# Performance work log

Hardware: AMD Instinct MI355X
Metric: run time of the kernel (lower is better)

The kernel has to match this reference:

```python
import jax, jax.numpy as jnp
import numpy as np

B, IN, OUT, M = 4096, 512, 512, 16


def setup_inputs() -> dict:
    key = jax.random.key(0)
    k1, k2, k3 = jax.random.split(key, 3)
    # inputs kept strictly positive and inside the physical range [0, 60]
    x = jax.random.uniform(k1, (B, IN), jnp.float32, 0.1, 10.0)
    # photonic basis coefficients: positive, with small polynomial terms
    b_coef = jax.random.uniform(k2, (M, 8), jnp.float32, 0.1, 0.9)
    b_coef = b_coef.at[:, 4:].multiply(0.01)
    coeffs = 0.01 * jax.random.normal(k3, (OUT, IN, M), jnp.float32)
    return {"x": x, "coeffs": coeffs, "b_coef": b_coef}


def _photonic_basis(x, b):
    # x: (B, IN) -> broadcast against M basis functions -> (B, IN, M)
    xe = x[:, :, None]                                   # (B, IN, 1)
    b1, b2, b3, b4, b5, b6, b7, b8 = [b[:, i][None, None, :] for i in range(8)]
    inner = jnp.expm1(b3 * xe)
    powered = jnp.power(inner, b4)
    y = (b1 * jnp.log(1.0 + b2 * jnp.log1p(powered))
         + b5 * xe + b6 * xe**2 + b7 * xe**3 + b8 * xe**4)
    return y


def reference(x, coeffs, b_coef):
    # basis: (B, IN, M); double reduce over (IN, M) == GEMM of size B x (IN*M) x OUT
    basis = _photonic_basis(x, b_coef)
    y = jnp.einsum('bim,oim->bo', basis, coeffs)         # (B, OUT)
    return y
```

## Files before the change

kernel.cpp:

```cpp
#include <hip/hip_runtime.h>
#include <hip/hip_bf16.h>
#include <stdint.h>

#define B_DIM   4096
#define IN_DIM  512
#define OUT_DIM 512
#define M_DIM   16
#define K_DIM   (IN_DIM * M_DIM)
#define MN      (B_DIM * OUT_DIM)

typedef unsigned short ushort_t;
typedef __attribute__((ext_vector_type(8))) __bf16 bf16x8;
typedef __attribute__((ext_vector_type(2))) __bf16 bf16x2;
typedef __attribute__((ext_vector_type(4))) float  f32x4;

__device__ __forceinline__ ushort_t f2bf(float f) {
  union { float f; uint32_t u; } v; v.f = f;
  uint32_t u = v.u + 0x7fffu + ((v.u >> 16) & 1u);
  return (ushort_t)(u >> 16);
}

__device__ __forceinline__ uint32_t pkbf(float lo, float hi) {
  union { bf16x2 h; uint32_t u; } v;
  v.h[0] = (__bf16)lo; v.h[1] = (__bf16)hi;
  return v.u;
}

__device__ __forceinline__ float rfl(float f) {
  union { float f; int i; } v; v.f = f;
  v.i = __builtin_amdgcn_readfirstlane(v.i);
  return v.f;
}

#define CONV_N4 (OUT_DIM * K_DIM / 4)
__global__ __launch_bounds__(256) void convert_coeffs_kernel(
    const float* __restrict__ src, ushort_t* __restrict__ dst) {
  int i = blockIdx.x * 256 + threadIdx.x;
  float4 v = ((const float4*)src)[i];
  ushort4 o;
  o.x = f2bf(v.x); o.y = f2bf(v.y); o.z = f2bf(v.z); o.w = f2bf(v.w);
  ((ushort4*)dst)[i] = o;
}

#define BM 128
#define BN 512
#define BK 32
#define SPLITK 8
#define KC (K_DIM / SPLITK)
#define NITER (KC / BK)
#define XCOLS (KC / M_DIM)
#define XPAD  129

#define GLD16(g, l) \
  __builtin_amdgcn_global_load_lds((const __attribute__((address_space(1))) void*)(g), \
                                   (__attribute__((address_space(3))) void*)(l), 16, 0, 0)

template <int ATOMIC>
__global__ __launch_bounds__(512, 2) void gemm_kernel(
    const float* __restrict__ x,
    const ushort_t* __restrict__ Bt,
    const float* __restrict__ bc,
    float* __restrict__ P) {
  __shared__ __align__(16) ushort_t As[2][BM * BK];
  __shared__ __align__(16) ushort_t Bs[2][BN * BK];
  __shared__ __align__(16) float    Xs[XCOLS * XPAD];
  const int tid  = threadIdx.x;
  const int wave = tid >> 6;
  const int lane = tid & 63;
  const int wgid = blockIdx.x;
  const int ks = wgid & 7, bm = wgid >> 3;

  {
    const int r = tid >> 2, q = tid & 3;
    const float4* xrow = (const float4*)(x + (size_t)(bm * BM + r) * IN_DIM + ks * XCOLS);
    #pragma unroll
    for (int j = 0; j < 4; ++j) {
      float4 v = xrow[q * 4 + j];
      Xs[(q * 16 + j * 4 + 0) * XPAD + r] = v.x;
      Xs[(q * 16 + j * 4 + 1) * XPAD + r] = v.y;
      Xs[(q * 16 + j * 4 + 2) * XPAD + r] = v.z;
      Xs[(q * 16 + j * 4 + 3) * XPAD + r] = v.w;
    }
  }

  const int srow = wave * 16 + (lane >> 2);
  const int scol = (((lane & 3) ^ ((lane >> 3) & 3)) * 8);
  const ushort_t* Bg0 = Bt + (size_t)srow * K_DIM + ks * KC + scol;
  const ushort_t* Bg1 = Bg0 + (size_t)128 * K_DIM;
  const ushort_t* Bg2 = Bg0 + (size_t)256 * K_DIM;
  const ushort_t* Bg3 = Bg0 + (size_t)384 * K_DIM;
  const int bofs0 = (wave * 16) * BK;
  const int bofs1 = (128 + wave * 16) * BK;
  const int bofs2 = (256 + wave * 16) * BK;
  const int bofs3 = (384 + wave * 16) * BK;

#define STAGEB(b) do { \
    GLD16(Bg0, &Bs[b][bofs0]); GLD16(Bg1, &Bs[b][bofs1]); \
    GLD16(Bg2, &Bs[b][bofs2]); GLD16(Bg3, &Bs[b][bofs3]); \
    Bg0 += BK; Bg1 += BK; Bg2 += BK; Bg3 += BK; } while (0)

  const int half = wave & 1;
  const int arow = (wave >> 1) * 32 + (lane >> 1);
  const int il   = lane & 1;
  const int aslot = ((il * 2 + half) ^ ((lane >> 2) & 3));
  const int awe   = arow * BK + aslot * 8;
  const int xbase = il * XPAD + arow;

  float c1[8], c2[8], c3[8], c4[8], c5[8], c6[8], c7[8], c8[8];
  {
    const float* bch = bc + half * 64;
    #pragma unroll
    for (int m = 0; m < 8; ++m) {
      c1[m] = rfl(bch[m*8+0]); c2[m] = rfl(bch[m*8+1]);
      c3[m] = rfl(bch[m*8+2]); c4[m] = rfl(bch[m*8+3]);
      c5[m] = rfl(bch[m*8+4]); c6[m] = rfl(bch[m*8+5]);
      c7[m] = rfl(bch[m*8+6]); c8[m] = rfl(bch[m*8+7]);
    }
  }

  const float LOG2E = 1.44269504088896340736f;
  const float LN2   = 0.69314718055994530942f;
#define BASIS(b, t) do { \
    float xv = Xs[xbase + 2 * XPAD * (t)]; \
    float xl2 = xv * LOG2E; \
    float x2 = xv * xv, x3 = x2 * xv, x4 = x2 * x2; \
    float ym[8]; \
    _Pragma("unroll") \
    for (int mi = 0; mi < 8; ++mi) { \
      float e     = __builtin_amdgcn_exp2f(c3[mi] * xl2); \
      float inner = e - 1.0f; \
      float p     = __builtin_amdgcn_exp2f(c4[mi] * __builtin_amdgcn_logf(inner)); \
      float u     = LN2 * __builtin_amdgcn_logf(1.0f + p); \
      float vv    = LN2 * __builtin_amdgcn_logf(1.0f + c2[mi] * u); \
      ym[mi] = c1[mi] * vv + c5[mi] * xv + c6[mi] * x2 + c7[mi] * x3 + c8[mi] * x4; \
    } \
    *(uint4*)&As[b][awe] = make_uint4(pkbf(ym[0], ym[1]), pkbf(ym[2], ym[3]), \
                                      pkbf(ym[4], ym[5]), pkbf(ym[6], ym[7])); \
  } while (0)

  const int wr = wave >> 2, wc = wave & 3;
  const int fm = lane & 15;
  const int fkswz = (((lane >> 4) ^ ((lane >> 1) & 3)) << 3);

  f32x4 acc[4][8] = {};

#define COMPUTE(b) do { \
    bf16x8 af[4], bfv[8]; \
    _Pragma("unroll") \
    for (int t2 = 0; t2 < 4; ++t2) \
      af[t2] = *(const bf16x8*)&As[b][(wr * 64 + t2 * 16 + fm) * BK + fkswz]; \
    _Pragma("unroll") \
    for (int u = 0; u < 8; ++u) \
      bfv[u] = *(const bf16x8*)&Bs[b][(wc * 128 + u * 16 + fm) * BK + fkswz]; \
    __builtin_amdgcn_s_setprio(1); \
    _Pragma("unroll") \
    for (int mt = 0; mt < 4; ++mt) \
      _Pragma("unroll") \
      for (int nt = 0; nt < 8; ++nt) \
        acc[mt][nt] = __builtin_amdgcn_mfma_f32_16x16x32_bf16(af[mt], bfv[nt], acc[mt][nt], 0, 0, 0); \
    __builtin_amdgcn_s_setprio(0); \
  } while (0)

  STAGEB(0);
  __syncthreads();
  BASIS(0, 0);
  __syncthreads();
  for (int kt = 0; kt < NITER - 2; kt += 2) {
    STAGEB(1); COMPUTE(0); BASIS(1, kt + 1);
    __syncthreads();
    STAGEB(0); COMPUTE(1); BASIS(0, kt + 2);
    __syncthreads();
  }
  STAGEB(1); COMPUTE(0); BASIS(1, NITER - 1);
  __syncthreads();
  COMPUTE(1);

  const int colb = wc * 128 + fm;
  const int rowb = bm * BM + wr * 64 + (lane >> 4) * 4;
  float* out = P + (ATOMIC ? (size_t)0 : (size_t)ks * MN);
  #pragma unroll
  for (int mt = 0; mt < 4; ++mt) {
    #pragma unroll
    for (int nt = 0; nt < 8; ++nt) {
      #pragma unroll
      for (int j = 0; j < 4; ++j) {
        int row = rowb + mt * 16 + j;
        int col = colb + nt * 16;
        float vv = acc[mt][nt][j];
        if (ATOMIC) atomicAdd(out + (size_t)row * OUT_DIM + col, vv);
        else        out[(size_t)row * OUT_DIM + col] = vv;
      }
    }
  }
#undef STAGEB
#undef BASIS
#undef COMPUTE
}

__global__ __launch_bounds__(256) void reduce_kernel(
    const float* __restrict__ P, float* __restrict__ out) {
  int i = blockIdx.x * 256 + threadIdx.x;
  const float4* p = (const float4*)P;
  float4 r = p[i];
  #pragma unroll
  for (int s = 1; s < SPLITK; ++s) {
    float4 v = p[i + (size_t)s * (MN / 4)];
    r.x += v.x; r.y += v.y; r.z += v.z; r.w += v.w;
  }
  ((float4*)out)[i] = r;
}

extern "C" void kernel_launch(void* const* d_in, const int* in_sizes, int n_in,
                              void* d_out, int out_size, void* d_ws, size_t ws_size,
                              hipStream_t stream) {
  const float* x      = (const float*)d_in[0];
  const float* coeffs = (const float*)d_in[1];
  const float* b_coef = (const float*)d_in[2];
  float* out = (float*)d_out;
  char*  ws  = (char*)d_ws;

  const size_t COEF_BYTES = (size_t)OUT_DIM * K_DIM * 2;
  ushort_t* coefb = (ushort_t*)ws;
  float* partials = (float*)(ws + COEF_BYTES);
  const size_t FULL = COEF_BYTES + (size_t)SPLITK * MN * 4;
  const bool use_atomic = (ws_size < FULL);

  convert_coeffs_kernel<<<CONV_N4 / 256, 256, 0, stream>>>(coeffs, coefb);

  const int nblk = (B_DIM / BM) * SPLITK;
  if (use_atomic) {
    hipMemsetAsync(d_out, 0, (size_t)MN * 4, stream);
    gemm_kernel<1><<<nblk, 512, 0, stream>>>(x, coefb, b_coef, out);
  } else {
    gemm_kernel<0><<<nblk, 512, 0, stream>>>(x, coefb, b_coef, partials);
    reduce_kernel<<<MN / 4 / 256, 256, 0, stream>>>(partials, out);
  }
}
```

Before: 140.4 us.

## Split output columns across two workgroups with 256-thread blocks

Halves the N tile from 512 to 256 and adds a column-block index, so each 256-thread workgroup computes a 128x256 output tile, which doubles the grid to 512 blocks. Each thread now evaluates two basis vectors per k-step instead of one, and the Xs padding is dropped. The goal is a smaller per-block footprint and more blocks for occupancy and load balance. The cost is that the expensive transcendental basis evaluation is now repeated by both column blocks, doubling that work overall.

```diff
diff --git a/kernel.cpp b/kernel.cpp
--- a/kernel.cpp
+++ b/kernel.cpp
@@ -43,72 +43,70 @@
 }
 
 #define BM 128
-#define BN 512
+#define BN 256
 #define BK 32
 #define SPLITK 8
 #define KC (K_DIM / SPLITK)
 #define NITER (KC / BK)
 #define XCOLS (KC / M_DIM)
-#define XPAD  129
 
 #define GLD16(g, l) \
   __builtin_amdgcn_global_load_lds((const __attribute__((address_space(1))) void*)(g), \
                                    (__attribute__((address_space(3))) void*)(l), 16, 0, 0)
 
 template <int ATOMIC>
-__global__ __launch_bounds__(512, 2) void gemm_kernel(
+__global__ __launch_bounds__(256, 2) void gemm_kernel(
     const float* __restrict__ x,
     const ushort_t* __restrict__ Bt,
     const float* __restrict__ bc,
     float* __restrict__ P) {
   __shared__ __align__(16) ushort_t As[2][BM * BK];
   __shared__ __align__(16) ushort_t Bs[2][BN * BK];
-  __shared__ __align__(16) float    Xs[XCOLS * XPAD];
+  __shared__ __align__(16) float    Xs[XCOLS * BM];
   const int tid  = threadIdx.x;
   const int wave = tid >> 6;
   const int lane = tid & 63;
   const int wgid = blockIdx.x;
-  const int ks = wgid & 7, bm = wgid >> 3;
+  const int ks = wgid & 7, bn = (wgid >> 3) & 1, bm = wgid >> 4;
 
   {
-    const int r = tid >> 2, q = tid & 3;
-    const float4* xrow = (const float4*)(x + (size_t)(bm * BM + r) * IN_DIM + ks * XCOLS);
+    const int r = tid >> 1, hf = tid & 1;
+    const float4* xr4 = (const float4*)(x + (size_t)(bm * BM + r) * IN_DIM + ks * XCOLS + hf * 32);
     #pragma unroll
-    for (int j = 0; j < 4; ++j) {
-      float4 v = xrow[q * 4 + j];
-      Xs[(q * 16 + j * 4 + 0) * XPAD + r] = v.x;
-      Xs[(q * 16 + j * 4 + 1) * XPAD + r] = v.y;
-      Xs[(q * 16 + j * 4 + 2) * XPAD + r] = v.z;
-      Xs[(q * 16 + j * 4 + 3) * XPAD + r] = v.w;
+    for (int j = 0; j < 8; ++j) {
+      float4 v = xr4[j];
+      Xs[(hf * 32 + j * 4 + 0) * BM + r] = v.x;
+      Xs[(hf * 32 + j * 4 + 1) * BM + r] = v.y;
+      Xs[(hf * 32 + j * 4 + 2) * BM + r] = v.z;
+      Xs[(hf * 32 + j * 4 + 3) * BM + r] = v.w;
     }
   }
 
   const int srow = wave * 16 + (lane >> 2);
   const int scol = (((lane & 3) ^ ((lane >> 3) & 3)) * 8);
-  const ushort_t* Bg0 = Bt + (size_t)srow * K_DIM + ks * KC + scol;
-  const ushort_t* Bg1 = Bg0 + (size_t)128 * K_DIM;
-  const ushort_t* Bg2 = Bg0 + (size_t)256 * K_DIM;
-  const ushort_t* Bg3 = Bg0 + (size_t)384 * K_DIM;
+  const ushort_t* Bg0 = Bt + (size_t)(bn * BN + srow) * K_DIM + ks * KC + scol;
+  const ushort_t* Bg1 = Bg0 + (size_t)64  * K_DIM;
+  const ushort_t* Bg2 = Bg0 + (size_t)128 * K_DIM;
+  const ushort_t* Bg3 = Bg0 + (size_t)192 * K_DIM;
   const int bofs0 = (wave * 16) * BK;
-  const int bofs1 = (128 + wave * 16) * BK;
-  const int bofs2 = (256 + wave * 16) * BK;
-  const int bofs3 = (384 + wave * 16) * BK;
+  const int bofs1 = (64  + wave * 16) * BK;
+  const int bofs2 = (128 + wave * 16) * BK;
+  const int bofs3 = (192 + wave * 16) * BK;
 
 #define STAGEB(b) do { \
     GLD16(Bg0, &Bs[b][bofs0]); GLD16(Bg1, &Bs[b][bofs1]); \
     GLD16(Bg2, &Bs[b][bofs2]); GLD16(Bg3, &Bs[b][bofs3]); \
     Bg0 += BK; Bg1 += BK; Bg2 += BK; Bg3 += BK; } while (0)
 
-  const int half = wave & 1;
-  const int arow = (wave >> 1) * 32 + (lane >> 1);
-  const int il   = lane & 1;
-  const int aslot = ((il * 2 + half) ^ ((lane >> 2) & 3));
-  const int awe   = arow * BK + aslot * 8;
-  const int xbase = il * XPAD + arow;
+  const int mh   = wave & 1;
+  const int xrow = (wave >> 1) * 64 + lane;
+  const int wsz  = (xrow >> 1) & 3;
+  const int aw0  = xrow * BK + ((mh ^ wsz) << 3);
+  const int aw1  = xrow * BK + (((2 + mh) ^ wsz) << 3);
 
   float c1[8], c2[8], c3[8], c4[8], c5[8], c6[8], c7[8], c8[8];
   {
-    const float* bch = bc + half * 64;
+    const float* bch = bc + mh * 64;
     #pragma unroll
     for (int m = 0; m < 8; ++m) {
       c1[m] = rfl(bch[m*8+0]); c2[m] = rfl(bch[m*8+1]);
@@ -120,10 +118,9 @@
 
   const float LOG2E = 1.44269504088896340736f;
   const float LN2   = 0.69314718055994530942f;
-#define BASIS(b, t) do { \
-    float xv = Xs[xbase + 2 * XPAD * (t)]; \
-    float xl2 = xv * LOG2E; \
-    float x2 = xv * xv, x3 = x2 * xv, x4 = x2 * x2; \
+#define BEVAL(xv, dst) do { \
+    float xl2 = (xv) * LOG2E; \
+    float x2 = (xv) * (xv), x3 = x2 * (xv), x4 = x2 * x2; \
     float ym[8]; \
     _Pragma("unroll") \
     for (int mi = 0; mi < 8; ++mi) { \
@@ -132,13 +129,20 @@
       float p     = __builtin_amdgcn_exp2f(c4[mi] * __builtin_amdgcn_logf(inner)); \
       float u     = LN2 * __builtin_amdgcn_logf(1.0f + p); \
       float vv    = LN2 * __builtin_amdgcn_logf(1.0f + c2[mi] * u); \
-      ym[mi] = c1[mi] * vv + c5[mi] * xv + c6[mi] * x2 + c7[mi] * x3 + c8[mi] * x4; \
+      ym[mi] = c1[mi] * vv + c5[mi] * (xv) + c6[mi] * x2 + c7[mi] * x3 + c8[mi] * x4; \
     } \
-    *(uint4*)&As[b][awe] = make_uint4(pkbf(ym[0], ym[1]), pkbf(ym[2], ym[3]), \
-                                      pkbf(ym[4], ym[5]), pkbf(ym[6], ym[7])); \
+    *(uint4*)(dst) = make_uint4(pkbf(ym[0], ym[1]), pkbf(ym[2], ym[3]), \
+                                pkbf(ym[4], ym[5]), pkbf(ym[6], ym[7])); \
   } while (0)
 
-  const int wr = wave >> 2, wc = wave & 3;
+#define BASIS(b, t) do { \
+    float xv0 = Xs[(2 * (t) + 0) * BM + xrow]; \
+    float xv1 = Xs[(2 * (t) + 1) * BM + xrow]; \
+    BEVAL(xv0, &As[b][aw0]); \
+    BEVAL(xv1, &As[b][aw1]); \
+  } while (0)
+
+  const int wr = wave >> 1, wc = wave & 1;
   const int fm = lane & 15;
   const int fkswz = (((lane >> 4) ^ ((lane >> 1) & 3)) << 3);
 
@@ -175,7 +179,7 @@
   __syncthreads();
   COMPUTE(1);
 
-  const int colb = wc * 128 + fm;
+  const int colb = bn * BN + wc * 128 + fm;
   const int rowb = bm * BM + wr * 64 + (lane >> 4) * 4;
   float* out = P + (ATOMIC ? (size_t)0 : (size_t)ks * MN);
   #pragma unroll
@@ -193,6 +197,7 @@
     }
   }
 #undef STAGEB
+#undef BEVAL
 #undef BASIS
 #undef COMPUTE
 }
@@ -227,12 +232,12 @@
 
   convert_coeffs_kernel<<<CONV_N4 / 256, 256, 0, stream>>>(coeffs, coefb);
 
-  const int nblk = (B_DIM / BM) * SPLITK;
+  const int nblk = (B_DIM / BM) * (OUT_DIM / BN) * SPLITK;
   if (use_atomic) {
     hipMemsetAsync(d_out, 0, (size_t)MN * 4, stream);
-    gemm_kernel<1><<<nblk, 512, 0, stream>>>(x, coefb, b_coef, out);
+    gemm_kernel<1><<<nblk, 256, 0, stream>>>(x, coefb, b_coef, out);
   } else {
-    gemm_kernel<0><<<nblk, 512, 0, stream>>>(x, coefb, b_coef, partials);
+    gemm_kernel<0><<<nblk, 256, 0, stream>>>(x, coefb, b_coef, partials);
     reduce_kernel<<<MN / 4 / 256, 256, 0, stream>>>(partials, out);
   }
 }
```

Result: slower. 154.4 us (+10.0%).

## Triple-buffer B tiles with prefetch distance two and explicit waitcnt barriers

Applied to the files above, without the earlier changes.

Moves the B-tile LDS staging from double to triple buffering, so global→LDS loads are issued two K-steps ahead. Each iteration now computes the next A basis tile before the MFMA block. `__syncthreads` is replaced by a manual `s_waitcnt vmcnt(4)` plus raw barrier, so the most recent prefetch can stay in flight. This costs about 32KB more LDS and relies on hand-counted vmcnt values, which is fragile if the load count changes.

```diff
diff --git a/kernel.cpp b/kernel.cpp
--- a/kernel.cpp
+++ b/kernel.cpp
@@ -55,6 +55,13 @@
   __builtin_amdgcn_global_load_lds((const __attribute__((address_space(1))) void*)(g), \
                                    (__attribute__((address_space(3))) void*)(l), 16, 0, 0)
 
+#define VMW_LGKM(N) do { \
+    asm volatile("s_waitcnt vmcnt(" #N ") lgkmcnt(0)" ::: "memory"); \
+    __builtin_amdgcn_sched_barrier(0); } while (0)
+#define RAW_BAR() do { \
+    __builtin_amdgcn_s_barrier(); \
+    __builtin_amdgcn_sched_barrier(0); } while (0)
+
 template <int ATOMIC>
 __global__ __launch_bounds__(512, 2) void gemm_kernel(
     const float* __restrict__ x,
@@ -62,7 +69,7 @@
     const float* __restrict__ bc,
     float* __restrict__ P) {
   __shared__ __align__(16) ushort_t As[2][BM * BK];
-  __shared__ __align__(16) ushort_t Bs[2][BN * BK];
+  __shared__ __align__(16) ushort_t Bs[3][BN * BK];
   __shared__ __align__(16) float    Xs[XCOLS * XPAD];
   const int tid  = threadIdx.x;
   const int wave = tid >> 6;
@@ -93,10 +100,12 @@
   const int bofs1 = (128 + wave * 16) * BK;
   const int bofs2 = (256 + wave * 16) * BK;
   const int bofs3 = (384 + wave * 16) * BK;
-
-#define STAGEB(b) do { \
-    GLD16(Bg0, &Bs[b][bofs0]); GLD16(Bg1, &Bs[b][bofs1]); \
-    GLD16(Bg2, &Bs[b][bofs2]); GLD16(Bg3, &Bs[b][bofs3]); \
+  ushort_t* const BsBase = &Bs[0][0];
+
+#define STAGEB(lb) do { \
+    ushort_t* bb = BsBase + (lb) * (BN * BK); \
+    GLD16(Bg0, bb + bofs0); GLD16(Bg1, bb + bofs1); \
+    GLD16(Bg2, bb + bofs2); GLD16(Bg3, bb + bofs3); \
     Bg0 += BK; Bg1 += BK; Bg2 += BK; Bg3 += BK; } while (0)
 
   const int half = wave & 1;
@@ -120,7 +129,7 @@
 
   const float LOG2E = 1.44269504088896340736f;
   const float LN2   = 0.69314718055994530942f;
-#define BASIS(b, t) do { \
+#define BASIS(pa, t) do { \
     float xv = Xs[xbase + 2 * XPAD * (t)]; \
     float xl2 = xv * LOG2E; \
     float x2 = xv * xv, x3 = x2 * xv, x4 = x2 * x2; \
@@ -134,8 +143,8 @@
       float vv    = LN2 * __builtin_amdgcn_logf(1.0f + c2[mi] * u); \
       ym[mi] = c1[mi] * vv + c5[mi] * xv + c6[mi] * x2 + c7[mi] * x3 + c8[mi] * x4; \
     } \
-    *(uint4*)&As[b][awe] = make_uint4(pkbf(ym[0], ym[1]), pkbf(ym[2], ym[3]), \
-                                      pkbf(ym[4], ym[5]), pkbf(ym[6], ym[7])); \
+    *(uint4*)((pa) + awe) = make_uint4(pkbf(ym[0], ym[1]), pkbf(ym[2], ym[3]), \
+                                       pkbf(ym[4], ym[5]), pkbf(ym[6], ym[7])); \
   } while (0)
 
   const int wr = wave >> 2, wc = wave & 3;
@@ -144,14 +153,15 @@
 
   f32x4 acc[4][8] = {};
 
-#define COMPUTE(b) do { \
+#define COMPUTE(pa, lb) do { \
+    const ushort_t* bb = BsBase + (lb) * (BN * BK); \
     bf16x8 af[4], bfv[8]; \
     _Pragma("unroll") \
     for (int t2 = 0; t2 < 4; ++t2) \
-      af[t2] = *(const bf16x8*)&As[b][(wr * 64 + t2 * 16 + fm) * BK + fkswz]; \
+      af[t2] = *(const bf16x8*)((pa) + (wr * 64 + t2 * 16 + fm) * BK + fkswz); \
     _Pragma("unroll") \
     for (int u = 0; u < 8; ++u) \
-      bfv[u] = *(const bf16x8*)&Bs[b][(wc * 128 + u * 16 + fm) * BK + fkswz]; \
+      bfv[u] = *(const bf16x8*)(bb + (wc * 128 + u * 16 + fm) * BK + fkswz); \
     __builtin_amdgcn_s_setprio(1); \
     _Pragma("unroll") \
     for (int mt = 0; mt < 4; ++mt) \
@@ -161,19 +171,27 @@
     __builtin_amdgcn_s_setprio(0); \
   } while (0)
 
-  STAGEB(0);
+  STAGEB(0); STAGEB(1);
   __syncthreads();
-  BASIS(0, 0);
-  __syncthreads();
-  for (int kt = 0; kt < NITER - 2; kt += 2) {
-    STAGEB(1); COMPUTE(0); BASIS(1, kt + 1);
-    __syncthreads();
-    STAGEB(0); COMPUTE(1); BASIS(0, kt + 2);
-    __syncthreads();
-  }
-  STAGEB(1); COMPUTE(0); BASIS(1, NITER - 1);
-  __syncthreads();
-  COMPUTE(1);
+  ushort_t* pAc = &As[0][0];
+  ushort_t* pAp = &As[1][0];
+  BASIS(pAc, 0);
+  VMW_LGKM(0); RAW_BAR();
+
+  int lb = 0, lbN = 2;
+  for (int t = 0; t < NITER - 2; ++t) {
+    STAGEB(lbN);
+    BASIS(pAp, t + 1);
+    COMPUTE(pAc, lb);
+    VMW_LGKM(4); RAW_BAR();
+    lb  = (lb  == 2) ? 0 : lb  + 1;
+    lbN = (lbN == 2) ? 0 : lbN + 1;
+    ushort_t* tmp = pAc; pAc = pAp; pAp = tmp;
+  }
+  BASIS(pAp, NITER - 1);
+  COMPUTE(pAc, lb);
+  VMW_LGKM(0); RAW_BAR();
+  COMPUTE(pAp, 1);
 
   const int colb = wc * 128 + fm;
   const int rowb = bm * BM + wr * 64 + (lane >> 4) * 4;
```

Measured after the change: 135.3 us. 1.04x faster.

## Triple-buffer B tiles with vmcnt-based barriers and fold LN2 into coefficients

Applied to the files above, without the earlier changes.

Grows the B shared-memory ring from two to three buffers so global-to-LDS loads run two k-steps ahead. The full __syncthreads is replaced by an inline s_waitcnt vmcnt(4)/s_barrier, which waits only for the older tile and leaves the newest prefetch in flight. The basis computation is moved ahead of the MFMA block in each step. The LN2 scaling is folded into the c1/c2 constants, removing two multiplies per basis element. This raises LDS use (roughly 145KB per block) and relies on the hand-written wait counts matching the number of outstanding loads.

```diff
diff --git a/kernel.cpp b/kernel.cpp
--- a/kernel.cpp
+++ b/kernel.cpp
@@ -55,6 +55,9 @@
   __builtin_amdgcn_global_load_lds((const __attribute__((address_space(1))) void*)(g), \
                                    (__attribute__((address_space(3))) void*)(l), 16, 0, 0)
 
+#define WAIT_BAR(N) \
+  asm volatile("s_waitcnt vmcnt(" #N ") lgkmcnt(0)\n\ts_barrier" ::: "memory")
+
 template <int ATOMIC>
 __global__ __launch_bounds__(512, 2) void gemm_kernel(
     const float* __restrict__ x,
@@ -62,7 +65,7 @@
     const float* __restrict__ bc,
     float* __restrict__ P) {
   __shared__ __align__(16) ushort_t As[2][BM * BK];
-  __shared__ __align__(16) ushort_t Bs[2][BN * BK];
+  __shared__ __align__(16) ushort_t Bs[3][BN * BK];
   __shared__ __align__(16) float    Xs[XCOLS * XPAD];
   const int tid  = threadIdx.x;
   const int wave = tid >> 6;
@@ -94,9 +97,9 @@
   const int bofs2 = (256 + wave * 16) * BK;
   const int bofs3 = (384 + wave * 16) * BK;
 
-#define STAGEB(b) do { \
-    GLD16(Bg0, &Bs[b][bofs0]); GLD16(Bg1, &Bs[b][bofs1]); \
-    GLD16(Bg2, &Bs[b][bofs2]); GLD16(Bg3, &Bs[b][bofs3]); \
+#define STAGEB(lb) do { \
+    GLD16(Bg0, &Bs[lb][bofs0]); GLD16(Bg1, &Bs[lb][bofs1]); \
+    GLD16(Bg2, &Bs[lb][bofs2]); GLD16(Bg3, &Bs[lb][bofs3]); \
     Bg0 += BK; Bg1 += BK; Bg2 += BK; Bg3 += BK; } while (0)
 
   const int half = wave & 1;
@@ -106,21 +109,21 @@
   const int awe   = arow * BK + aslot * 8;
   const int xbase = il * XPAD + arow;
 
+  const float LOG2E = 1.44269504088896340736f;
+  const float LN2   = 0.69314718055994530942f;
   float c1[8], c2[8], c3[8], c4[8], c5[8], c6[8], c7[8], c8[8];
   {
     const float* bch = bc + half * 64;
     #pragma unroll
     for (int m = 0; m < 8; ++m) {
-      c1[m] = rfl(bch[m*8+0]); c2[m] = rfl(bch[m*8+1]);
+      c1[m] = rfl(rfl(bch[m*8+0]) * LN2); c2[m] = rfl(rfl(bch[m*8+1]) * LN2);
       c3[m] = rfl(bch[m*8+2]); c4[m] = rfl(bch[m*8+3]);
       c5[m] = rfl(bch[m*8+4]); c6[m] = rfl(bch[m*8+5]);
       c7[m] = rfl(bch[m*8+6]); c8[m] = rfl(bch[m*8+7]);
     }
   }
 
-  const float LOG2E = 1.44269504088896340736f;
-  const float LN2   = 0.69314718055994530942f;
-#define BASIS(b, t) do { \
+#define BASIS(ab, t) do { \
     float xv = Xs[xbase + 2 * XPAD * (t)]; \
     float xl2 = xv * LOG2E; \
     float x2 = xv * xv, x3 = x2 * xv, x4 = x2 * x2; \
@@ -130,12 +133,12 @@
       float e     = __builtin_amdgcn_exp2f(c3[mi] * xl2); \
       float inner = e - 1.0f; \
       float p     = __builtin_amdgcn_exp2f(c4[mi] * __builtin_amdgcn_logf(inner)); \
-      float u     = LN2 * __builtin_amdgcn_logf(1.0f + p); \
-      float vv    = LN2 * __builtin_amdgcn_logf(1.0f + c2[mi] * u); \
+      float L1    = __builtin_amdgcn_logf(1.0f + p); \
+      float vv    = __builtin_amdgcn_logf(1.0f + c2[mi] * L1); \
       ym[mi] = c1[mi] * vv + c5[mi] * xv + c6[mi] * x2 + c7[mi] * x3 + c8[mi] * x4; \
     } \
-    *(uint4*)&As[b][awe] = make_uint4(pkbf(ym[0], ym[1]), pkbf(ym[2], ym[3]), \
-                                      pkbf(ym[4], ym[5]), pkbf(ym[6], ym[7])); \
+    *(uint4*)(&As[ab][awe]) = make_uint4(pkbf(ym[0], ym[1]), pkbf(ym[2], ym[3]), \
+                                         pkbf(ym[4], ym[5]), pkbf(ym[6], ym[7])); \
   } while (0)
 
   const int wr = wave >> 2, wc = wave & 3;
@@ -144,14 +147,14 @@
 
   f32x4 acc[4][8] = {};
 
-#define COMPUTE(b) do { \
+#define COMPUTE(ab, lb) do { \
     bf16x8 af[4], bfv[8]; \
     _Pragma("unroll") \
     for (int t2 = 0; t2 < 4; ++t2) \
-      af[t2] = *(const bf16x8*)&As[b][(wr * 64 + t2 * 16 + fm) * BK + fkswz]; \
+      af[t2] = *(const bf16x8*)&As[ab][(wr * 64 + t2 * 16 + fm) * BK + fkswz]; \
     _Pragma("unroll") \
     for (int u = 0; u < 8; ++u) \
-      bfv[u] = *(const bf16x8*)&Bs[b][(wc * 128 + u * 16 + fm) * BK + fkswz]; \
+      bfv[u] = *(const bf16x8*)&Bs[lb][(wc * 128 + u * 16 + fm) * BK + fkswz]; \
     __builtin_amdgcn_s_setprio(1); \
     _Pragma("unroll") \
     for (int mt = 0; mt < 4; ++mt) \
@@ -161,19 +164,26 @@
     __builtin_amdgcn_s_setprio(0); \
   } while (0)
 
-  STAGEB(0);
+#define STEP(lbN, ap, ac, lb, t1) do { \
+    STAGEB(lbN); BASIS(ap, t1); COMPUTE(ac, lb); WAIT_BAR(4); } while (0)
+
+  STAGEB(0); STAGEB(1);
   __syncthreads();
   BASIS(0, 0);
-  __syncthreads();
-  for (int kt = 0; kt < NITER - 2; kt += 2) {
-    STAGEB(1); COMPUTE(0); BASIS(1, kt + 1);
-    __syncthreads();
-    STAGEB(0); COMPUTE(1); BASIS(0, kt + 2);
-    __syncthreads();
-  }
-  STAGEB(1); COMPUTE(0); BASIS(1, NITER - 1);
-  __syncthreads();
-  COMPUTE(1);
+  WAIT_BAR(0);
+
+  for (int tb = 0; tb < NITER - 2; tb += 6) {
+    STEP(2, 1, 0, 0, tb + 1);
+    STEP(0, 0, 1, 1, tb + 2);
+    STEP(1, 1, 0, 2, tb + 3);
+    STEP(2, 0, 1, 0, tb + 4);
+    STEP(0, 1, 0, 1, tb + 5);
+    STEP(1, 0, 1, 2, tb + 6);
+  }
+  BASIS(1, NITER - 1);
+  COMPUTE(0, 0);
+  WAIT_BAR(0);
+  COMPUTE(1, 1);
 
   const int colb = wc * 128 + fm;
   const int rowb = bm * BM + wr * 64 + (lane >> 4) * 4;
@@ -195,6 +205,7 @@
 #undef STAGEB
 #undef BASIS
 #undef COMPUTE
+#undef STEP
 }
 
 __global__ __launch_bounds__(256) void reduce_kernel(
```

After: 135.0 us. -3.8%, faster.
